# Kernel optimization log

Hardware: AMD Instinct MI355X
Metric: run time of the kernel (lower is better)

## Reference

```python
import jax, jax.numpy as jnp
import numpy as np
from jax import lax

B, C, H, W = 32, 64, 64, 64
O, KH, KW = 128, 3, 3
LAT = 64


def setup_inputs() -> dict:
    key = jax.random.key(0)
    ks = jax.random.split(key, 4)
    x = jax.random.normal(ks[0], (B, C, H, W), dtype=jnp.float32)
    W1 = jax.random.normal(ks[1], (LAT, LAT), dtype=jnp.float32) * (1.0 / np.sqrt(LAT))
    b1 = jnp.zeros((LAT,), dtype=jnp.float32)
    W2 = jax.random.normal(ks[2], (LAT, LAT), dtype=jnp.float32) * (1.0 / np.sqrt(LAT))
    b2 = jnp.zeros((LAT,), dtype=jnp.float32)
    Wf = jax.random.normal(ks[3], (LAT, O * C * KH * KW), dtype=jnp.float32) * (1.0 / np.sqrt(LAT))
    bf = jnp.zeros((O * C * KH * KW,), dtype=jnp.float32)
    return {"x": x, "W1": W1, "b1": b1, "W2": W2, "b2": b2, "Wf": Wf, "bf": bf}


def reference(x, W1, b1, W2, b2, Wf, bf):
    b, c, h, w = x.shape
    # adaptive_avg_pool2d(x, (1,1)) -> global average pool -> [B, C]
    gap = x.mean(axis=(2, 3))
    # kernel generator MLP (C == latent_dim, so no extra projection)
    f = jax.nn.relu(gap @ W1 + b1)
    f = jax.nn.relu(f @ W2 + b2)
    kernels = (f @ Wf + bf).reshape(b, O, c, KH, KW)  # per-sample conv kernels
    # batched dynamic-weight conv as a single grouped convolution (groups=B)
    xg = x.reshape(1, b * c, h, w)                 # [1, B*C, H, W]
    kg = kernels.reshape(b * O, c, KH, KW)         # [B*O, C, KH, KW]
    out = lax.conv_general_dilated(
        xg, kg,
        window_strides=(1, 1),
        padding=[(1, 1), (1, 1)],
        feature_group_count=b,
        dimension_numbers=("NCHW", "OIHW", "NCHW"),
    )
    return out.reshape(b, O, h, w)
```

## Files before the change

### kernel.cpp

```cpp
#include <hip/hip_runtime.h>

#define B_  32
#define C_  64
#define H_  64
#define W_  64
#define O_  128
#define LAT 64
#define HW  (H_*W_)
#define KJ  (O_*C_*9)
#define KTOT 576
#define NKS 18

typedef __bf16 bf16x8 __attribute__((ext_vector_type(8)));
typedef float  f32x4  __attribute__((ext_vector_type(4)));

__global__ __launch_bounds__(256) void transpose_gap(const float* __restrict__ x,
                                                     __bf16* __restrict__ xT,
                                                     float* __restrict__ gap_part) {
    int bh = blockIdx.x, b = bh >> 6, h = bh & 63;
    __shared__ float lt[64 * 65];
    int t = threadIdx.x;
    int cc0 = t >> 4, w4 = (t & 15) * 4;

    #pragma unroll
    for (int i = 0; i < 4; i++) {
        int cc = cc0 + 16 * i;
        float4 v = *(const float4*)(x + (((size_t)(b * C_ + cc) * H_) + h) * W_ + w4);
        lt[cc * 65 + w4 + 0] = v.x;
        lt[cc * 65 + w4 + 1] = v.y;
        lt[cc * 65 + w4 + 2] = v.z;
        lt[cc * 65 + w4 + 3] = v.w;
        float s = (v.x + v.y) + (v.z + v.w);
        s += __shfl_xor(s, 1); s += __shfl_xor(s, 2);
        s += __shfl_xor(s, 4); s += __shfl_xor(s, 8);
        if ((t & 15) == 0) gap_part[h * 2048 + b * 64 + cc] = s;
    }
    __syncthreads();

    __bf16* dst = xT + ((size_t)(b * H_ + h) * W_) * C_;
    #pragma unroll
    for (int k = 0; k < 2; k++) {
        int chunk = t + k * 256;
        int w = chunk >> 3, c8 = chunk & 7;
        __bf16 g[8];
        #pragma unroll
        for (int i = 0; i < 8; i++) g[i] = (__bf16)lt[(c8 * 8 + i) * 65 + w];
        *(int4*)(dst + w * C_ + c8 * 8) = *(int4*)g;
    }
}

__global__ __launch_bounds__(64) void mlp_kernel(const float* __restrict__ gap_part,
                                                 const float* __restrict__ W1,
                                                 const float* __restrict__ b1,
                                                 const float* __restrict__ W2,
                                                 const float* __restrict__ b2,
                                                 float* __restrict__ f2t) {
    int b = blockIdx.x, j = threadIdx.x;
    float s = 0.f;
    #pragma unroll 16
    for (int h = 0; h < 64; h++) s += gap_part[h * 2048 + b * 64 + j];
    __shared__ float g[LAT], f1[LAT];
    g[j] = s * (1.0f / (float)HW);
    __syncthreads();
    float acc = b1[j];
    #pragma unroll 8
    for (int l = 0; l < LAT; l++) acc = fmaf(g[l], W1[l * LAT + j], acc);
    f1[j] = fmaxf(acc, 0.f);
    __syncthreads();
    float acc2 = b2[j];
    #pragma unroll 8
    for (int l = 0; l < LAT; l++) acc2 = fmaf(f1[l], W2[l * LAT + j], acc2);
    f2t[j * B_ + b] = fmaxf(acc2, 0.f);
}

#define KGP2 592
__global__ __launch_bounds__(576) void kergen_kernel(const float* __restrict__ f2t,
                                                     const float* __restrict__ Wf,
                                                     const float* __restrict__ bfv,
                                                     __bf16* __restrict__ kbf2) {
    int o = blockIdx.x & 127, b0 = (blockIdx.x >> 7) * 16;
    int t = threadIdx.x;
    __shared__ __bf16 ltk[16 * KGP2];

    int j = o * KTOT + t;
    float acc[16];
    float base = bfv[j];
    #pragma unroll
    for (int i = 0; i < 16; i++) acc[i] = base;

    for (int l8 = 0; l8 < LAT; l8 += 8) {
        float w8[8];
        #pragma unroll
        for (int i = 0; i < 8; i++) w8[i] = Wf[(size_t)(l8 + i) * KJ + j];
        #pragma unroll
        for (int i = 0; i < 8; i++) {
            #pragma unroll
            for (int bb = 0; bb < 16; bb++)
                acc[bb] = fmaf(f2t[(l8 + i) * B_ + b0 + bb], w8[i], acc[bb]);
        }
    }

    int c = t / 9, tap = t - c * 9;
    int tpp = (tap * 2 + (c >> 5)) * 32 + (c & 31);
    #pragma unroll
    for (int bb = 0; bb < 16; bb++) ltk[bb * KGP2 + tpp] = (__bf16)acc[bb];
    __syncthreads();
    int ks = t >> 5, kk = t & 31;
    #pragma unroll
    for (int bb = 0; bb < 16; bb++)
        kbf2[(((size_t)(b0 + bb) * NKS + ks) * O_ + o) * 32 + kk] = ltk[bb * KGP2 + t];
}

#define CPAD 72
#define ROWE (66 * CPAD)

__global__ __launch_bounds__(256, 3) void conv_mfma(const __bf16* __restrict__ xT,
                                                    const __bf16* __restrict__ kbf2,
                                                    float* __restrict__ out) {
    int b  = blockIdx.y;
    int bx = blockIdx.x;
    int htile = (bx & 7) * 4 + (bx >> 3);
    int h0 = htile * 2;
    __shared__ __bf16 xs[4 * ROWE];
    int tid = threadIdx.x;

    if (tid < 64) {
        int r = tid >> 4, which = (tid >> 3) & 1, c8 = tid & 7;
        *(int4*)(xs + (r * 66 + which * 65) * CPAD + c8 * 8) = int4{0, 0, 0, 0};
    }
    if (h0 == 0) {
        for (int i = tid; i < ROWE / 8; i += 256)
            *(int4*)(xs + i * 8) = int4{0, 0, 0, 0};
    }
    if (h0 == H_ - 2) {
        for (int i = tid; i < ROWE / 8; i += 256)
            *(int4*)(xs + 3 * ROWE + i * 8) = int4{0, 0, 0, 0};
    }

    #pragma unroll
    for (int i = 0; i < 8; i++) {
        int chunk = tid + i * 256;
        int c8 = chunk & 7, w = (chunk >> 3) & 63, r = chunk >> 9;
        int hh = h0 - 1 + r;
        if ((unsigned)hh < (unsigned)H_) {
            int4 v = *(const int4*)(xT + ((size_t)(b * H_ + hh) * W_ + w) * C_ + c8 * 8);
            *(int4*)(xs + (r * 66 + w + 1) * CPAD + c8 * 8) = v;
        }
    }
    __syncthreads();

    int wave = tid >> 6, lane = tid & 63;
    int wi = wave >> 1, wj = wave & 1;
    int l15 = lane & 15, quad = lane >> 4;

    const __bf16* kbA = kbf2 + (size_t)b * (NKS * O_ * 32);
    int mrow = wi * 64 + l15;

    f32x4 acc[4][4];
    #pragma unroll
    for (int mt = 0; mt < 4; mt++)
        #pragma unroll
        for (int nt = 0; nt < 4; nt++)
            acc[mt][nt] = (f32x4){0.f, 0.f, 0.f, 0.f};

    bf16x8 Abuf[3][4];
    #pragma unroll
    for (int d = 0; d < 2; d++)
        #pragma unroll
        for (int mt = 0; mt < 4; mt++)
            Abuf[d][mt] = *(const bf16x8*)(kbA + d * (O_ * 32) +
                                           (mrow + mt * 16) * 32 + quad * 8);

    #pragma unroll
    for (int ks = 0; ks < NKS; ks++) {
        if (ks < NKS - 2) {
            #pragma unroll
            for (int mt = 0; mt < 4; mt++)
                Abuf[(ks + 2) % 3][mt] = *(const bf16x8*)(kbA + (ks + 2) * (O_ * 32) +
                                                          (mrow + mt * 16) * 32 + quad * 8);
        }
        int tap = ks >> 1;
        int kh = tap / 3, kw = tap - kh * 3;
        int c0 = (ks & 1) * 32;
        const __bf16* Bb = xs + ((wj + kh) * 66 + kw + l15) * CPAD + c0 + quad * 8;
        #pragma unroll
        for (int nt = 0; nt < 4; nt++) {
            bf16x8 bfrag = *(const bf16x8*)(Bb + nt * 16 * CPAD);
            #pragma unroll
            for (int mt = 0; mt < 4; mt++)
                acc[mt][nt] = __builtin_amdgcn_mfma_f32_16x16x32_bf16(
                    Abuf[ks % 3][mt], bfrag, acc[mt][nt], 0, 0, 0);
        }
    }

    int h = h0 + wj;
    float* ob = out + ((size_t)b * O_ + wi * 64) * HW + h * W_;
    #pragma unroll
    for (int mt = 0; mt < 4; mt++) {
        #pragma unroll
        for (int nt = 0; nt < 4; nt++) {
            int w = nt * 16 + l15;
            #pragma unroll
            for (int r = 0; r < 4; r++) {
                int oo = mt * 16 + quad * 4 + r;
                ob[(size_t)oo * HW + w] = acc[mt][nt][r];
            }
        }
    }
}

extern "C" void kernel_launch(void* const* d_in, const int* in_sizes, int n_in,
                              void* d_out, int out_size, void* d_ws, size_t ws_size,
                              hipStream_t stream) {
    const float* x  = (const float*)d_in[0];
    const float* W1 = (const float*)d_in[1];
    const float* b1 = (const float*)d_in[2];
    const float* W2 = (const float*)d_in[3];
    const float* b2 = (const float*)d_in[4];
    const float* Wf = (const float*)d_in[5];
    const float* bf = (const float*)d_in[6];
    float* out = (float*)d_out;

    float*  gap_part = (float*)d_ws;
    float*  f2t      = (float*)((char*)d_ws + 524288);
    __bf16* kbf2     = (__bf16*)((char*)d_ws + 540672);
    __bf16* xT       = (__bf16*)((char*)d_ws + 540672 + (size_t)B_ * NKS * O_ * 32 * 2);

    transpose_gap<<<B_ * H_, 256, 0, stream>>>(x, xT, gap_part);
    mlp_kernel<<<B_, 64, 0, stream>>>(gap_part, W1, b1, W2, b2, f2t);
    kergen_kernel<<<256, 576, 0, stream>>>(f2t, Wf, bf, kbf2);
    conv_mfma<<<dim3(32, B_), 256, 0, stream>>>(xT, kbf2, out);
}
```

Baseline: 149.7 us.

## Fuse MLP into kernel generator and make conv persistent with deeper prefetch

Folds the GAP-reduce and two-layer MLP into the kernel-generator kernel, so each block recomputes the MLP for its 16 samples and one launch is removed. The conv kernel becomes a grid-stride loop over 1024 tiles using 768 blocks, and its A-fragment prefetch goes from two stages ahead to three. The fused kernel repeats the MLP work 128 times per sample group. The 768-block grid with 1024 tiles leaves a second partial wave, and the extra prefetch buffer raises register pressure.

```diff
diff --git a/kernel.cpp b/kernel.cpp
--- a/kernel.cpp
+++ b/kernel.cpp
@@ -49,38 +49,58 @@
     }
 }
 
-__global__ __launch_bounds__(64) void mlp_kernel(const float* __restrict__ gap_part,
-                                                 const float* __restrict__ W1,
-                                                 const float* __restrict__ b1,
-                                                 const float* __restrict__ W2,
-                                                 const float* __restrict__ b2,
-                                                 float* __restrict__ f2t) {
-    int b = blockIdx.x, j = threadIdx.x;
-    float s = 0.f;
-    #pragma unroll 16
-    for (int h = 0; h < 64; h++) s += gap_part[h * 2048 + b * 64 + j];
-    __shared__ float g[LAT], f1[LAT];
-    g[j] = s * (1.0f / (float)HW);
-    __syncthreads();
-    float acc = b1[j];
-    #pragma unroll 8
-    for (int l = 0; l < LAT; l++) acc = fmaf(g[l], W1[l * LAT + j], acc);
-    f1[j] = fmaxf(acc, 0.f);
-    __syncthreads();
-    float acc2 = b2[j];
-    #pragma unroll 8
-    for (int l = 0; l < LAT; l++) acc2 = fmaf(f1[l], W2[l * LAT + j], acc2);
-    f2t[j * B_ + b] = fmaxf(acc2, 0.f);
-}
-
 #define KGP2 592
-__global__ __launch_bounds__(576) void kergen_kernel(const float* __restrict__ f2t,
-                                                     const float* __restrict__ Wf,
-                                                     const float* __restrict__ bfv,
-                                                     __bf16* __restrict__ kbf2) {
+__global__ __launch_bounds__(576) void kergen_fused(const float* __restrict__ gap_part,
+                                                    const float* __restrict__ W1,
+                                                    const float* __restrict__ b1,
+                                                    const float* __restrict__ W2,
+                                                    const float* __restrict__ b2,
+                                                    const float* __restrict__ Wf,
+                                                    const float* __restrict__ bfv,
+                                                    __bf16* __restrict__ kbf2) {
     int o = blockIdx.x & 127, b0 = (blockIdx.x >> 7) * 16;
     int t = threadIdx.x;
+    __shared__ float gL[16 * 64];
+    __shared__ float f1L[16 * 64];
+    __shared__ float f2T[64 * 16];
     __shared__ __bf16 ltk[16 * KGP2];
+
+    int bb1 = t >> 6, c = t & 63;
+    if (t < 512) {
+        float s0 = 0.f, s1 = 0.f;
+        #pragma unroll 8
+        for (int h = 0; h < 64; h++) {
+            s0 += gap_part[h * 2048 + (b0 + bb1) * 64 + c];
+            s1 += gap_part[h * 2048 + (b0 + 8 + bb1) * 64 + c];
+        }
+        gL[bb1 * 64 + c] = s0 * (1.0f / (float)HW);
+        gL[(bb1 + 8) * 64 + c] = s1 * (1.0f / (float)HW);
+    }
+    __syncthreads();
+    if (t < 512) {
+        float a1 = b1[c], a2 = a1;
+        #pragma unroll 8
+        for (int l = 0; l < LAT; l++) {
+            float w = W1[l * LAT + c];
+            a1 = fmaf(gL[bb1 * 64 + l], w, a1);
+            a2 = fmaf(gL[(bb1 + 8) * 64 + l], w, a2);
+        }
+        f1L[bb1 * 64 + c] = fmaxf(a1, 0.f);
+        f1L[(bb1 + 8) * 64 + c] = fmaxf(a2, 0.f);
+    }
+    __syncthreads();
+    if (t < 512) {
+        float a1 = b2[c], a2 = a1;
+        #pragma unroll 8
+        for (int l = 0; l < LAT; l++) {
+            float w = W2[l * LAT + c];
+            a1 = fmaf(f1L[bb1 * 64 + l], w, a1);
+            a2 = fmaf(f1L[(bb1 + 8) * 64 + l], w, a2);
+        }
+        f2T[c * 16 + bb1] = fmaxf(a1, 0.f);
+        f2T[c * 16 + bb1 + 8] = fmaxf(a2, 0.f);
+    }
+    __syncthreads();
 
     int j = o * KTOT + t;
     float acc[16];
@@ -94,21 +114,24 @@
         for (int i = 0; i < 8; i++) w8[i] = Wf[(size_t)(l8 + i) * KJ + j];
         #pragma unroll
         for (int i = 0; i < 8; i++) {
+            const float* fp = &f2T[(l8 + i) * 16];
             #pragma unroll
             for (int bb = 0; bb < 16; bb++)
-                acc[bb] = fmaf(f2t[(l8 + i) * B_ + b0 + bb], w8[i], acc[bb]);
-        }
-    }
-
-    int c = t / 9, tap = t - c * 9;
-    int tpp = (tap * 2 + (c >> 5)) * 32 + (c & 31);
+                acc[bb] = fmaf(fp[bb], w8[i], acc[bb]);
+        }
+    }
+
+    int cc = t / 9, tap = t - cc * 9;
+    int tpp = (tap * 2 + (cc >> 5)) * 32 + (cc & 31);
     #pragma unroll
     for (int bb = 0; bb < 16; bb++) ltk[bb * KGP2 + tpp] = (__bf16)acc[bb];
     __syncthreads();
-    int ks = t >> 5, kk = t & 31;
-    #pragma unroll
-    for (int bb = 0; bb < 16; bb++)
-        kbf2[(((size_t)(b0 + bb) * NKS + ks) * O_ + o) * 32 + kk] = ltk[bb * KGP2 + t];
+    #pragma unroll
+    for (int bb = 0; bb < 16; bb++) {
+        int ks = t >> 5;
+        kbf2[(((size_t)(b0 + bb) * NKS + ks) * O_ + o) * 32 + (t & 31)] =
+            ltk[bb * KGP2 + t];
+    }
 }
 
 #define CPAD 72
@@ -117,93 +140,96 @@
 __global__ __launch_bounds__(256, 3) void conv_mfma(const __bf16* __restrict__ xT,
                                                     const __bf16* __restrict__ kbf2,
                                                     float* __restrict__ out) {
-    int b  = blockIdx.y;
-    int bx = blockIdx.x;
-    int htile = (bx & 7) * 4 + (bx >> 3);
-    int h0 = htile * 2;
     __shared__ __bf16 xs[4 * ROWE];
     int tid = threadIdx.x;
-
-    if (tid < 64) {
-        int r = tid >> 4, which = (tid >> 3) & 1, c8 = tid & 7;
-        *(int4*)(xs + (r * 66 + which * 65) * CPAD + c8 * 8) = int4{0, 0, 0, 0};
-    }
-    if (h0 == 0) {
-        for (int i = tid; i < ROWE / 8; i += 256)
-            *(int4*)(xs + i * 8) = int4{0, 0, 0, 0};
-    }
-    if (h0 == H_ - 2) {
-        for (int i = tid; i < ROWE / 8; i += 256)
-            *(int4*)(xs + 3 * ROWE + i * 8) = int4{0, 0, 0, 0};
-    }
-
-    #pragma unroll
-    for (int i = 0; i < 8; i++) {
-        int chunk = tid + i * 256;
-        int c8 = chunk & 7, w = (chunk >> 3) & 63, r = chunk >> 9;
-        int hh = h0 - 1 + r;
-        if ((unsigned)hh < (unsigned)H_) {
-            int4 v = *(const int4*)(xT + ((size_t)(b * H_ + hh) * W_ + w) * C_ + c8 * 8);
-            *(int4*)(xs + (r * 66 + w + 1) * CPAD + c8 * 8) = v;
-        }
-    }
-    __syncthreads();
-
     int wave = tid >> 6, lane = tid & 63;
     int wi = wave >> 1, wj = wave & 1;
     int l15 = lane & 15, quad = lane >> 4;
 
-    const __bf16* kbA = kbf2 + (size_t)b * (NKS * O_ * 32);
-    int mrow = wi * 64 + l15;
-
-    f32x4 acc[4][4];
-    #pragma unroll
-    for (int mt = 0; mt < 4; mt++)
-        #pragma unroll
-        for (int nt = 0; nt < 4; nt++)
-            acc[mt][nt] = (f32x4){0.f, 0.f, 0.f, 0.f};
-
-    bf16x8 Abuf[3][4];
-    #pragma unroll
-    for (int d = 0; d < 2; d++)
+    for (int tile = blockIdx.x; tile < 1024; tile += 768) {
+        int b = tile >> 5, bx = tile & 31;
+        int htile = (bx & 7) * 4 + (bx >> 3);
+        int h0 = htile * 2;
+
+        const __bf16* kbA = kbf2 + (size_t)b * (NKS * O_ * 32);
+        int mrow = wi * 64 + l15;
+
+        __syncthreads();
+
+        bf16x8 Abuf[4][4];
+        #pragma unroll
+        for (int d = 0; d < 3; d++)
+            #pragma unroll
+            for (int mt = 0; mt < 4; mt++)
+                Abuf[d][mt] = *(const bf16x8*)(kbA + d * (O_ * 32) +
+                                               (mrow + mt * 16) * 32 + quad * 8);
+
+        if (tid < 64) {
+            int r = tid >> 4, which = (tid >> 3) & 1, c8 = tid & 7;
+            *(int4*)(xs + (r * 66 + which * 65) * CPAD + c8 * 8) = int4{0, 0, 0, 0};
+        }
+        if (h0 == 0) {
+            for (int i = tid; i < ROWE / 8; i += 256)
+                *(int4*)(xs + i * 8) = int4{0, 0, 0, 0};
+        }
+        if (h0 == H_ - 2) {
+            for (int i = tid; i < ROWE / 8; i += 256)
+                *(int4*)(xs + 3 * ROWE + i * 8) = int4{0, 0, 0, 0};
+        }
+        #pragma unroll
+        for (int i = 0; i < 8; i++) {
+            int chunk = tid + i * 256;
+            int c8 = chunk & 7, w = (chunk >> 3) & 63, r = chunk >> 9;
+            int hh = h0 - 1 + r;
+            if ((unsigned)hh < (unsigned)H_) {
+                int4 v = *(const int4*)(xT + ((size_t)(b * H_ + hh) * W_ + w) * C_ + c8 * 8);
+                *(int4*)(xs + (r * 66 + w + 1) * CPAD + c8 * 8) = v;
+            }
+        }
+        __syncthreads();
+
+        f32x4 acc[4][4];
         #pragma unroll
         for (int mt = 0; mt < 4; mt++)
-            Abuf[d][mt] = *(const bf16x8*)(kbA + d * (O_ * 32) +
-                                           (mrow + mt * 16) * 32 + quad * 8);
-
-    #pragma unroll
-    for (int ks = 0; ks < NKS; ks++) {
-        if (ks < NKS - 2) {
-            #pragma unroll
-            for (int mt = 0; mt < 4; mt++)
-                Abuf[(ks + 2) % 3][mt] = *(const bf16x8*)(kbA + (ks + 2) * (O_ * 32) +
-                                                          (mrow + mt * 16) * 32 + quad * 8);
-        }
-        int tap = ks >> 1;
-        int kh = tap / 3, kw = tap - kh * 3;
-        int c0 = (ks & 1) * 32;
-        const __bf16* Bb = xs + ((wj + kh) * 66 + kw + l15) * CPAD + c0 + quad * 8;
-        #pragma unroll
-        for (int nt = 0; nt < 4; nt++) {
-            bf16x8 bfrag = *(const bf16x8*)(Bb + nt * 16 * CPAD);
-            #pragma unroll
-            for (int mt = 0; mt < 4; mt++)
-                acc[mt][nt] = __builtin_amdgcn_mfma_f32_16x16x32_bf16(
-                    Abuf[ks % 3][mt], bfrag, acc[mt][nt], 0, 0, 0);
-        }
-    }
-
-    int h = h0 + wj;
-    float* ob = out + ((size_t)b * O_ + wi * 64) * HW + h * W_;
-    #pragma unroll
-    for (int mt = 0; mt < 4; mt++) {
-        #pragma unroll
-        for (int nt = 0; nt < 4; nt++) {
-            int w = nt * 16 + l15;
-            #pragma unroll
-            for (int r = 0; r < 4; r++) {
-                int oo = mt * 16 + quad * 4 + r;
-                ob[(size_t)oo * HW + w] = acc[mt][nt][r];
+            #pragma unroll
+            for (int nt = 0; nt < 4; nt++)
+                acc[mt][nt] = (f32x4){0.f, 0.f, 0.f, 0.f};
+
+        #pragma unroll
+        for (int ks = 0; ks < NKS; ks++) {
+            if (ks < NKS - 3) {
+                #pragma unroll
+                for (int mt = 0; mt < 4; mt++)
+                    Abuf[(ks + 3) & 3][mt] =
+                        *(const bf16x8*)(kbA + (ks + 3) * (O_ * 32) +
+                                         (mrow + mt * 16) * 32 + quad * 8);
+            }
+            int tap = ks >> 1;
+            int kh = tap / 3, kw = tap - kh * 3;
+            int c0 = (ks & 1) * 32;
+            const __bf16* Bb = xs + ((wj + kh) * 66 + kw + l15) * CPAD + c0 + quad * 8;
+            #pragma unroll
+            for (int nt = 0; nt < 4; nt++) {
+                bf16x8 bfrag = *(const bf16x8*)(Bb + nt * 16 * CPAD);
+                #pragma unroll
+                for (int mt = 0; mt < 4; mt++)
+                    acc[mt][nt] = __builtin_amdgcn_mfma_f32_16x16x32_bf16(
+                        Abuf[ks & 3][mt], bfrag, acc[mt][nt], 0, 0, 0);
+            }
+        }
+
+        int h = h0 + wj;
+        float* ob = out + ((size_t)b * O_ + wi * 64) * HW + h * W_;
+        #pragma unroll
+        for (int mt = 0; mt < 4; mt++) {
+            #pragma unroll
+            for (int nt = 0; nt < 4; nt++) {
+                int w = nt * 16 + l15;
+                #pragma unroll
+                for (int r = 0; r < 4; r++) {
+                    int oo = mt * 16 + quad * 4 + r;
+                    ob[(size_t)oo * HW + w] = acc[mt][nt][r];
+                }
             }
         }
     }
@@ -222,12 +248,10 @@
     float* out = (float*)d_out;
 
     float*  gap_part = (float*)d_ws;
-    float*  f2t      = (float*)((char*)d_ws + 524288);
-    __bf16* kbf2     = (__bf16*)((char*)d_ws + 540672);
-    __bf16* xT       = (__bf16*)((char*)d_ws + 540672 + (size_t)B_ * NKS * O_ * 32 * 2);
+    __bf16* kbf2     = (__bf16*)((char*)d_ws + 524288);
+    __bf16* xT       = (__bf16*)((char*)d_ws + 524288 + (size_t)B_ * NKS * O_ * 32 * 2);
 
     transpose_gap<<<B_ * H_, 256, 0, stream>>>(x, xT, gap_part);
-    mlp_kernel<<<B_, 64, 0, stream>>>(gap_part, W1, b1, W2, b2, f2t);
-    kergen_kernel<<<256, 576, 0, stream>>>(f2t, Wf, bf, kbf2);
-    conv_mfma<<<dim3(32, B_), 256, 0, stream>>>(xT, kbf2, out);
-}
+    kergen_fused<<<256, 576, 0, stream>>>(gap_part, W1, b1, W2, b2, Wf, bf, kbf2);
+    conv_mfma<<<768, 256, 0, stream>>>(xT, kbf2, out);
+}
```

After: 213.8 us. 1.43x slower.
